# Kernel tuning notes

Measured on AMD Instinct MI355X. Metric: run time of the kernel, lower is better.

## Reference

```python
import jax, jax.numpy as jnp
import numpy as np

S, B, E, D, H, F, L = 1024, 8, 768, 8, 8, 2048, 4
D = 1024  # HIDDEN_DIM
H = 8     # nhead
DH = D // H
EPS = 1e-5


def _ln(x, g, b):
    m = jnp.mean(x, -1, keepdims=True)
    v = jnp.mean(jnp.square(x - m), -1, keepdims=True)
    return (x - m) * jax.lax.rsqrt(v + EPS) * g + b


def setup_inputs() -> dict:
    key = jax.random.key(0)
    ks = iter(jax.random.split(key, 16))
    n = lambda shape: jax.random.normal(next(ks), shape, jnp.float32) * 0.02
    return dict(
        x=jax.random.normal(next(ks), (S, B, E), jnp.float32),
        enc_w=n((D, E)), enc_b=jnp.zeros((D,), jnp.float32),
        enc_ln_g=jnp.ones((D,), jnp.float32), enc_ln_b=jnp.zeros((D,), jnp.float32),
        qkv_w=n((L, 3 * D, D)), qkv_b=jnp.zeros((L, 3 * D), jnp.float32),
        out_w=n((L, D, D)), out_b=jnp.zeros((L, D), jnp.float32),
        ln1_g=jnp.ones((L, D), jnp.float32), ln1_b=jnp.zeros((L, D), jnp.float32),
        ff1_w=n((L, F, D)), ff1_b=jnp.zeros((L, F), jnp.float32),
        ff2_w=n((L, D, F)), ff2_b=jnp.zeros((L, D), jnp.float32),
        ln2_g=jnp.ones((L, D), jnp.float32), ln2_b=jnp.zeros((L, D), jnp.float32),
        dec_w1=n((D // 2, D)), dec_b1=jnp.zeros((D // 2,), jnp.float32),
        dec_ln_g=jnp.ones((D // 2,), jnp.float32), dec_ln_b=jnp.zeros((D // 2,), jnp.float32),
        dec_w2=n((E, D // 2)), dec_b2=jnp.zeros((E,), jnp.float32),
    )


def reference(x, enc_w, enc_b, enc_ln_g, enc_ln_b, qkv_w, qkv_b, out_w, out_b,
              ln1_g, ln1_b, ff1_w, ff1_b, ff2_w, ff2_b, ln2_g, ln2_b,
              dec_w1, dec_b1, dec_ln_g, dec_ln_b, dec_w2, dec_b2):
    # encoder MLP: Linear -> LayerNorm -> ReLU (dropout = identity at eval)
    h = jax.nn.relu(_ln(x @ enc_w.T + enc_b, enc_ln_g, enc_ln_b))  # (S,B,D)
    scale = np.float32(1.0 / np.sqrt(DH))
    for l in range(L):  # 4 post-norm TransformerEncoderLayers, eager attention
        qkv = h @ qkv_w[l].T + qkv_b[l]                    # (S,B,3D)
        q, k, v = jnp.split(qkv, 3, axis=-1)
        q = q.reshape(S, B, H, DH)
        k = k.reshape(S, B, H, DH)
        v = v.reshape(S, B, H, DH)
        scores = jnp.einsum('sbhd,tbhd->bhst', q, k) * scale  # (B,H,S,S)
        p = jax.nn.softmax(scores, axis=-1)
        o = jnp.einsum('bhst,tbhd->sbhd', p, v).reshape(S, B, D)
        o = o @ out_w[l].T + out_b[l]
        h = _ln(h + o, ln1_g[l], ln1_b[l])
        f = jax.nn.relu(h @ ff1_w[l].T + ff1_b[l]) @ ff2_w[l].T + ff2_b[l]
        h = _ln(h + f, ln2_g[l], ln2_b[l])
    # decoder MLP
    d = jax.nn.relu(_ln(h @ dec_w1.T + dec_b1, dec_ln_g, dec_ln_b))
    return d @ dec_w2.T + dec_b2  # (S,B,E)
```

## Files before the change

### kernel.cpp

```cpp
#include <hip/hip_runtime.h>
#include <math.h>

#define S_ 1024
#define B_ 8
#define E_ 768
#define D_ 1024
#define H_ 8
#define F_ 2048
#define L_ 4
#define M_ (S_*B_)

typedef unsigned short u16;
typedef unsigned int u32;
typedef u16 u16x8 __attribute__((ext_vector_type(8)));
typedef u16 u16x4 __attribute__((ext_vector_type(4)));
typedef u16 u16x2 __attribute__((ext_vector_type(2)));
typedef u32 u32x2 __attribute__((ext_vector_type(2)));
typedef short bf16x8 __attribute__((ext_vector_type(8)));
typedef float f32x4 __attribute__((ext_vector_type(4)));

#define AS1 __attribute__((address_space(1)))
#define AS3 __attribute__((address_space(3)))

#define QSCALE 0.127517432f

__device__ __forceinline__ void gload_lds16(const void* g, void* l) {
  __builtin_amdgcn_global_load_lds((const AS1 void*)g, (AS3 void*)l, 16, 0, 0);
}
__device__ __forceinline__ u16 f2bf(float f) {
  unsigned u = __builtin_bit_cast(unsigned, f);
  return (u16)((u + 0x7fffu + ((u >> 16) & 1u)) >> 16);
}
__device__ __forceinline__ float bf2f(u16 h) {
  unsigned u = ((unsigned)h) << 16;
  return __builtin_bit_cast(float, u);
}
__device__ __forceinline__ u32 cvtpk(float a, float b) {
  u32 r;
  asm("v_cvt_pk_bf16_f32 %0, %1, %2" : "=v"(r) : "v"(a), "v"(b));
  return r;
}

__global__ __launch_bounds__(256) void conv4(
    const float* __restrict__ s0, u16* __restrict__ d0, int n0,
    const float* __restrict__ s1, u16* __restrict__ d1, int n1,
    const float* __restrict__ s2, u16* __restrict__ d2, int n2,
    const float* __restrict__ s3, u16* __restrict__ d3, int n3)
{
  int total = (n0 + n1 + n2 + n3) >> 2;
  for (int i = blockIdx.x * 256 + threadIdx.x; i < total; i += gridDim.x * 256) {
    int e = i << 2;
    const float* s; u16* d; int off;
    if (e < n0)           { s = s0; d = d0; off = e; }
    else if (e < n0+n1)   { s = s1; d = d1; off = e - n0; }
    else if (e < n0+n1+n2){ s = s2; d = d2; off = e - n0 - n1; }
    else                  { s = s3; d = d3; off = e - n0 - n1 - n2; }
    float4 v = *(const float4*)&s[off];
    u16x4 o; o[0]=f2bf(v.x); o[1]=f2bf(v.y); o[2]=f2bf(v.z); o[3]=f2bf(v.w);
    *(u16x4*)&d[off] = o;
  }
}

template<int ACT, int SCQ>
__global__ __launch_bounds__(512) void gemm512(
    const u16* __restrict__ A, const u16* __restrict__ W,
    const float* __restrict__ bias, u16* __restrict__ Cout,
    int M, int N, int K)
{
  __shared__ u16 lds[65536];
  const int gx = gridDim.x, nwg = gx * gridDim.y;
  const int lin = blockIdx.y * gx + blockIdx.x;
  const int work = (lin & 7) * (nwg >> 3) + (lin >> 3);
  const int bm = (work / gx) * 256, bn = (work % gx) * 256;
  const int tid = threadIdx.x;
  const int l = tid & 63;
  const int w = tid >> 6;
  const int l15 = l & 15, lg = l >> 4;
  const int wr = w >> 2, wc = w & 3;
  f32x4 acc[8][4] = {};
  const int nt = K >> 6;

#define STG(c, k0)                                                          \
  {                                                                         \
    u16* Ab = lds + (c)*32768;                                              \
    u16* Bb = Ab + 16384;                                                   \
    _Pragma("unroll")                                                       \
    for (int u = 0; u < 4; ++u) {                                           \
      int row = u*64 + (tid >> 3);                                          \
      int cb  = (tid & 7) ^ (row & 7);                                      \
      gload_lds16(A + (size_t)(bm + row) * K + (k0) + cb*8,                 \
                  Ab + u*4096 + tid*8);                                     \
    }                                                                       \
    _Pragma("unroll")                                                       \
    for (int u = 0; u < 4; ++u) {                                           \
      int row = u*64 + (tid >> 3);                                          \
      int cb  = (tid & 7) ^ (row & 7);                                      \
      gload_lds16(W + (size_t)(bn + row) * K + (k0) + cb*8,                 \
                  Bb + u*4096 + tid*8);                                     \
    }                                                                       \
  }

  STG(0, 0);
  STG(1, 64);
  asm volatile("s_waitcnt vmcnt(8)" ::: "memory");
  __builtin_amdgcn_s_barrier();

  for (int t = 0; t < nt; ++t) {
    const u16* Ab = lds + (t & 1)*32768;
    const u16* Bb = Ab + 16384;

    bf16x8 af[8], bfv[4];
    #pragma unroll
    for (int mi = 0; mi < 8; ++mi) {
      int row = wr*128 + mi*16 + l15;
      af[mi] = *(const bf16x8*)&Ab[row*64 + ((lg) ^ (row & 7))*8];
    }
    #pragma unroll
    for (int ni = 0; ni < 4; ++ni) {
      int row = wc*64 + ni*16 + l15;
      bfv[ni] = *(const bf16x8*)&Bb[row*64 + ((lg) ^ (row & 7))*8];
    }
    asm volatile("s_waitcnt lgkmcnt(0)" ::: "memory");
    __builtin_amdgcn_sched_barrier(0);
    #pragma unroll
    for (int mi = 0; mi < 8; ++mi)
      #pragma unroll
      for (int ni = 0; ni < 4; ++ni)
        acc[mi][ni] = __builtin_amdgcn_mfma_f32_16x16x32_bf16(af[mi], bfv[ni], acc[mi][ni], 0, 0, 0);

    #pragma unroll
    for (int mi = 0; mi < 8; ++mi) {
      int row = wr*128 + mi*16 + l15;
      af[mi] = *(const bf16x8*)&Ab[row*64 + ((4 + lg) ^ (row & 7))*8];
    }
    #pragma unroll
    for (int ni = 0; ni < 4; ++ni) {
      int row = wc*64 + ni*16 + l15;
      bfv[ni] = *(const bf16x8*)&Bb[row*64 + ((4 + lg) ^ (row & 7))*8];
    }
    asm volatile("s_waitcnt lgkmcnt(0)" ::: "memory");
    __builtin_amdgcn_sched_barrier(0);
    __builtin_amdgcn_s_barrier();

    if (t + 2 < nt) STG(t & 1, (t + 2) << 6);

    #pragma unroll
    for (int mi = 0; mi < 8; ++mi)
      #pragma unroll
      for (int ni = 0; ni < 4; ++ni)
        acc[mi][ni] = __builtin_amdgcn_mfma_f32_16x16x32_bf16(af[mi], bfv[ni], acc[mi][ni], 0, 0, 0);

    if (t + 1 < nt) {
      if (t + 2 < nt) { asm volatile("s_waitcnt vmcnt(8)" ::: "memory"); }
      else            { asm volatile("s_waitcnt vmcnt(0)" ::: "memory"); }
      __builtin_amdgcn_s_barrier();
    }
  }
#undef STG

  #pragma unroll
  for (int ni = 0; ni < 4; ++ni) {
    int col = bn + wc*64 + ni*16 + l15;
    float bv = bias[col];
    #pragma unroll
    for (int mi = 0; mi < 8; ++mi) {
      #pragma unroll
      for (int rr = 0; rr < 4; ++rr) {
        int row = bm + wr*128 + mi*16 + lg*4 + rr;
        float v = acc[mi][ni][rr] + bv;
        if (ACT) v = fmaxf(v, 0.f);
        if (SCQ) { if (col < 1024) v *= QSCALE; }
        Cout[(size_t)row * N + col] = f2bf(v);
      }
    }
  }
}

template<int ACT, int OUTBF, int SCQ, int RES>
__global__ __launch_bounds__(512) void gemm256(
    const u16* __restrict__ A, const u16* __restrict__ W,
    const float* __restrict__ bias, const u16* __restrict__ Rres,
    void* __restrict__ Cout, int M, int N, int K)
{
  __shared__ u16 lds[73728];
  const int gx = gridDim.x, nwg = gx * gridDim.y;
  const int lin = blockIdx.y * gx + blockIdx.x;
  const int work = (lin & 7) * (nwg >> 3) + (lin >> 3);
  const int bm = (work / gx) * 256, bn = (work % gx) * 128;
  const int tid = threadIdx.x;
  const int l = tid & 63;
  const int w = tid >> 6;
  const int l15 = l & 15, lg = l >> 4;
  const int wr = w >> 2, wc = w & 3;
  const int srow = tid >> 3;
  const int scb  = tid & 7;

  f32x4 acc[8][2] = {};
  const int nt = K >> 6;

#define STAGE_A(c, k0)                                                      \
  {                                                                         \
    u16* Ab = lds + (c)*24576;                                              \
    _Pragma("unroll")                                                       \
    for (int u = 0; u < 4; ++u) {                                           \
      int row = u*64 + srow;                                                \
      int cb  = scb ^ (row & 7);                                            \
      gload_lds16(A + (size_t)(bm + row) * K + (k0) + cb*8,                 \
                  Ab + u*4096 + tid*8);                                     \
    }                                                                       \
  }
#define STAGE_B(c, k0)                                                      \
  {                                                                         \
    u16* Bb = lds + (c)*24576 + 16384;                                      \
    _Pragma("unroll")                                                       \
    for (int u = 0; u < 2; ++u) {                                           \
      int row = u*64 + srow;                                                \
      int cb  = scb ^ (row & 7);                                            \
      gload_lds16(W + (size_t)(bn + row) * K + (k0) + cb*8,                 \
                  Bb + u*4096 + tid*8);                                     \
    }                                                                       \
  }

  STAGE_A(0, 0);  STAGE_B(0, 0);
  STAGE_A(1, 64); STAGE_B(1, 64);
  asm volatile("s_waitcnt vmcnt(6)" ::: "memory");
  __builtin_amdgcn_s_barrier();

  int cr = 0, cw = 2;
  for (int t = 0; t < nt; ++t) {
    const u16* Ab = lds + cr*24576;
    const u16* Bb = Ab + 16384;

    bf16x8 bfr[2][2];
    #pragma unroll
    for (int ni = 0; ni < 2; ++ni) {
      int row = wc*32 + ni*16 + l15;
      bfr[ni][0] = *(const bf16x8*)&Bb[row*64 + ((lg) ^ (row & 7))*8];
      bfr[ni][1] = *(const bf16x8*)&Bb[row*64 + ((4 + lg) ^ (row & 7))*8];
    }

    {
      bf16x8 af[4][2];
      #pragma unroll
      for (int mi = 0; mi < 4; ++mi) {
        int row = wr*128 + mi*16 + l15;
        af[mi][0] = *(const bf16x8*)&Ab[row*64 + ((lg) ^ (row & 7))*8];
        af[mi][1] = *(const bf16x8*)&Ab[row*64 + ((4 + lg) ^ (row & 7))*8];
      }
      if (t + 2 < nt) STAGE_A(cw, (t + 2) << 6);
      #pragma unroll
      for (int ks = 0; ks < 2; ++ks)
        #pragma unroll
        for (int mi = 0; mi < 4; ++mi)
          #pragma unroll
          for (int ni = 0; ni < 2; ++ni)
            acc[mi][ni] = __builtin_amdgcn_mfma_f32_16x16x32_bf16(af[mi][ks], bfr[ni][ks], acc[mi][ni], 0, 0, 0);
    }

    {
      bf16x8 af[4][2];
      #pragma unroll
      for (int mi = 0; mi < 4; ++mi) {
        int row = wr*128 + (4 + mi)*16 + l15;
        af[mi][0] = *(const bf16x8*)&Ab[row*64 + ((lg) ^ (row & 7))*8];
        af[mi][1] = *(const bf16x8*)&Ab[row*64 + ((4 + lg) ^ (row & 7))*8];
      }
      if (t + 2 < nt) STAGE_B(cw, (t + 2) << 6);
      #pragma unroll
      for (int ks = 0; ks < 2; ++ks)
        #pragma unroll
        for (int mi = 0; mi < 4; ++mi)
          #pragma unroll
          for (int ni = 0; ni < 2; ++ni)
            acc[4 + mi][ni] = __builtin_amdgcn_mfma_f32_16x16x32_bf16(af[mi][ks], bfr[ni][ks], acc[4 + mi][ni], 0, 0, 0);
    }

    if (t + 1 < nt) {
      if (t + 2 < nt) { asm volatile("s_waitcnt vmcnt(6)" ::: "memory"); }
      else            { asm volatile("s_waitcnt vmcnt(0)" ::: "memory"); }
      __builtin_amdgcn_s_barrier();
    }
    cr = (cr == 2) ? 0 : cr + 1;
    cw = (cw == 2) ? 0 : cw + 1;
  }
#undef STAGE_A
#undef STAGE_B

  u16* Cb = (u16*)Cout; float* Cf = (float*)Cout;
  #pragma unroll
  for (int ni = 0; ni < 2; ++ni) {
    int col = bn + wc*32 + ni*16 + l15;
    float bv = bias[col];
    #pragma unroll
    for (int mi = 0; mi < 8; ++mi) {
      #pragma unroll
      for (int rr = 0; rr < 4; ++rr) {
        int row = bm + wr*128 + mi*16 + lg*4 + rr;
        float v = acc[mi][ni][rr] + bv;
        if (RES) v += bf2f(Rres[(size_t)row * N + col]);
        if (ACT) v = fmaxf(v, 0.f);
        if (SCQ) { if (col < 1024) v *= QSCALE; }
        if (OUTBF) Cb[(size_t)row * N + col] = f2bf(v);
        else       Cf[(size_t)row * N + col] = v;
      }
    }
  }
}

template<int NV, bool RELU>
__global__ __launch_bounds__(256) void ln_bf16(
    const u16* __restrict__ X,
    const float* __restrict__ g, const float* __restrict__ b,
    u16* __restrict__ Y)
{
  constexpr int D = NV * 256;
  __shared__ float sbuf[8];
  const int tid = threadIdx.x;
  const size_t base = (size_t)blockIdx.x * D + tid * NV;
  float v[NV];
  if constexpr (NV == 4) {
    u16x4 xv = *(const u16x4*)&X[base];
    #pragma unroll
    for (int i = 0; i < 4; ++i) v[i] = bf2f(xv[i]);
  } else {
    u16x2 xv = *(const u16x2*)&X[base];
    #pragma unroll
    for (int i = 0; i < 2; ++i) v[i] = bf2f(xv[i]);
  }
  float sum = 0.f, sq = 0.f;
  #pragma unroll
  for (int i = 0; i < NV; ++i) { sum += v[i]; sq += v[i]*v[i]; }
  #pragma unroll
  for (int off = 32; off > 0; off >>= 1) {
    sum += __shfl_down(sum, off);
    sq  += __shfl_down(sq, off);
  }
  if ((tid & 63) == 0) { sbuf[tid >> 6] = sum; sbuf[4 + (tid >> 6)] = sq; }
  __syncthreads();
  sum = sbuf[0] + sbuf[1] + sbuf[2] + sbuf[3];
  sq  = sbuf[4] + sbuf[5] + sbuf[6] + sbuf[7];
  const float mean = sum / (float)D;
  const float rstd = rsqrtf(sq / (float)D - mean*mean + 1e-5f);
  const int c0 = tid * NV;
  if constexpr (NV == 4) {
    u16x4 o;
    #pragma unroll
    for (int i = 0; i < 4; ++i) {
      float t = (v[i] - mean) * rstd * g[c0+i] + b[c0+i];
      if (RELU) t = fmaxf(t, 0.f);
      o[i] = f2bf(t);
    }
    *(u16x4*)&Y[base] = o;
  } else {
    u16x2 o;
    #pragma unroll
    for (int i = 0; i < 2; ++i) {
      float t = (v[i] - mean) * rstd * g[c0+i] + b[c0+i];
      if (RELU) t = fmaxf(t, 0.f);
      o[i] = f2bf(t);
    }
    *(u16x2*)&Y[base] = o;
  }
}

__global__ __launch_bounds__(256) void vtrans(
    const u16* __restrict__ QKV, u16* __restrict__ Vt)
{
  __shared__ u16 Ls[32*132];
  const int st = blockIdx.x, bh = blockIdx.y;
  const int bb = bh >> 3, hh = bh & 7;
  const int t = threadIdx.x;
  #pragma unroll
  for (int i = 0; i < 2; ++i) {
    int e = i*256 + t;
    int s = e >> 4, d0 = (e & 15) * 8;
    u16x8 v = *(const u16x8*)&QKV[(size_t)((st*32 + s)*8 + bb)*3072 + 2048 + hh*128 + d0];
    #pragma unroll
    for (int j = 0; j < 4; ++j) {
      u16x2 p; p[0] = v[2*j]; p[1] = v[2*j+1];
      *(u16x2*)&Ls[s*132 + d0 + 2*j] = p;
    }
  }
  __syncthreads();
  #pragma unroll
  for (int i = 0; i < 2; ++i) {
    int e = i*256 + t;
    int d = e >> 2, s0 = (e & 3) * 8;
    u16x8 v;
    #pragma unroll
    for (int j = 0; j < 8; ++j) v[j] = Ls[(s0+j)*132 + d];
    *(u16x8*)&Vt[(size_t)bh*131072 + (size_t)d*1024 + st*32 + s0] = v;
  }
}

__global__ __launch_bounds__(512, 4) void attn_mfma(
    const u16* __restrict__ QKV, const u16* __restrict__ Vt,
    u16* __restrict__ AO)
{
  __shared__ u16 Ks[2][64*128];
  __shared__ u16 Vs[2][128*64];
  __shared__ u16 Pl[8][16*64];
  const int bid = blockIdx.x;
  const int wg = (bid & 7) * 64 + (bid >> 3);
  const int qt = wg & 7, bh = wg >> 3;
  const int bb = bh >> 3, hh = bh & 7;
  const int tid = threadIdx.x, w = tid >> 6, l = tid & 63;
  const int l15 = l & 15, lg = l >> 4;

  bf16x8 aq[4];
  {
    int q = qt*128 + w*16 + l15;
    const u16* qp = QKV + (size_t)(q*8 + bb)*3072 + hh*128 + lg*8;
    #pragma unroll
    for (int kc = 0; kc < 4; ++kc)
      aq[kc] = *(const bf16x8*)(qp + kc*32);
  }
  const u16* vbase = Vt + (size_t)bh*131072;

#define STAGE_KV(c, kt)                                                     \
  {                                                                         \
    _Pragma("unroll")                                                       \
    for (int i = 0; i < 2; ++i) {                                           \
      int e = (w*2 + i) * 512 + l * 8;                                      \
      int krow = e >> 7, d0 = e & 127;                                      \
      int dsw = d0 ^ ((krow & 7) << 3);                                     \
      gload_lds16(QKV + (size_t)(((kt)*64 + krow)*8 + bb)*3072 + 1024       \
                      + hh*128 + dsw,                                       \
                  &Ks[c][(w*2 + i) * 512]);                                 \
      int vd = e >> 6, vc = e & 63;                                         \
      int vsw = vc ^ ((vd & 7) << 3);                                       \
      gload_lds16(vbase + (size_t)vd*1024 + (kt)*64 + vsw,                  \
                  &Vs[c][(w*2 + i) * 512]);                                 \
    }                                                                       \
  }

  f32x4 of[8] = {};
  float mreg = -INFINITY, lpart = 0.f;
  const int psw = (l15 & 7) << 3;

  STAGE_KV(0, 0);
  __syncthreads();

  for (int kt = 0; kt < 16; ++kt) {
    const int cur = kt & 1;
    if (kt + 1 < 16) STAGE_KV(cur ^ 1, kt + 1);

    f32x4 sf[4] = {};
    #pragma unroll
    for (int kc = 0; kc < 4; ++kc) {
      #pragma unroll
      for (int f = 0; f < 4; ++f) {
        int krow = f*16 + l15;
        bf16x8 bk = *(const bf16x8*)&Ks[cur][krow*128 + ((kc*32 + lg*8) ^ ((krow & 7) << 3))];
        sf[f] = __builtin_amdgcn_mfma_f32_16x16x32_bf16(bk, aq[kc], sf[f], 0, 0, 0);
      }
    }

    float pm01 = fmaxf(fmaxf(sf[0][0], sf[0][1]), fmaxf(sf[0][2], sf[0][3]));
    float pm23 = fmaxf(fmaxf(sf[1][0], sf[1][1]), fmaxf(sf[1][2], sf[1][3]));
    float pm45 = fmaxf(fmaxf(sf[2][0], sf[2][1]), fmaxf(sf[2][2], sf[2][3]));
    float pm67 = fmaxf(fmaxf(sf[3][0], sf[3][1]), fmaxf(sf[3][2], sf[3][3]));
    float pmax = fmaxf(fmaxf(pm01, pm23), fmaxf(pm45, pm67));
    pmax = fmaxf(pmax, __shfl_xor(pmax, 16));
    pmax = fmaxf(pmax, __shfl_xor(pmax, 32));

    if (__any(pmax > mreg + 8.f)) {
      float mn = fmaxf(mreg, pmax);
      float al = exp2f(mreg - mn);
      mreg = mn;
      lpart *= al;
      #pragma unroll
      for (int r = 0; r < 4; ++r) {
        float alq = __shfl(al, (l & 48) + lg*4 + r);
        #pragma unroll
        for (int ni = 0; ni < 8; ++ni) of[ni][r] *= alq;
      }
    }

    float psum = 0.f;
    #pragma unroll
    for (int f = 0; f < 4; ++f) {
      float p0 = exp2f(sf[f][0] - mreg);
      float p1 = exp2f(sf[f][1] - mreg);
      float p2 = exp2f(sf[f][2] - mreg);
      float p3 = exp2f(sf[f][3] - mreg);
      psum += (p0 + p1) + (p2 + p3);
      u32x2 pk; pk[0] = cvtpk(p0, p1); pk[1] = cvtpk(p2, p3);
      *(u32x2*)&Pl[w][l15*64 + ((f*16 + lg*4) ^ psw)] = pk;
    }
    lpart += psum;

    bf16x8 pa0 = *(const bf16x8*)&Pl[w][l15*64 + ((lg*8) ^ psw)];
    bf16x8 pa1 = *(const bf16x8*)&Pl[w][l15*64 + ((32 + lg*8) ^ psw)];
    #pragma unroll
    for (int ni = 0; ni < 8; ++ni) {
      int n = ni*16 + l15;
      int nsw = (n & 7) << 3;
      bf16x8 vb0 = *(const bf16x8*)&Vs[cur][n*64 + ((lg*8) ^ nsw)];
      bf16x8 vb1 = *(const bf16x8*)&Vs[cur][n*64 + ((32 + lg*8) ^ nsw)];
      of[ni] = __builtin_amdgcn_mfma_f32_16x16x32_bf16(pa0, vb0, of[ni], 0, 0, 0);
      of[ni] = __builtin_amdgcn_mfma_f32_16x16x32_bf16(pa1, vb1, of[ni], 0, 0, 0);
    }

    if (kt + 1 < 16) __syncthreads();
  }
#undef STAGE_KV

  float ls = lpart;
  ls += __shfl_xor(ls, 16);
  ls += __shfl_xor(ls, 32);
  float inv = 1.f / ls;
  #pragma unroll
  for (int r = 0; r < 4; ++r) {
    float invq = __shfl(inv, (l & 48) + lg*4 + r);
    int q = qt*128 + w*16 + lg*4 + r;
    size_t base = (size_t)(q*8 + bb) * 1024 + hh*128;
    #pragma unroll
    for (int ni = 0; ni < 8; ++ni)
      AO[base + ni*16 + l15] = f2bf(of[ni][r] * invq);
  }
}

#define O_WENC  0ull
#define O_WDEC1 786432ull
#define O_WDEC2 1310720ull
#define O_WLQ   1703936ull
#define O_WLO   4849664ull
#define O_WLF1  5898240ull
#define O_WLF2  7995392ull
#define O_R     10092544ull
#define O_H     35258368ull
#define O_AO    43646976ull
#define O_VT    52035584ull

extern "C" void kernel_launch(void* const* d_in, const int* in_sizes, int n_in,
                              void* d_out, int out_size, void* d_ws, size_t ws_size,
                              hipStream_t stream) {
  (void)in_sizes; (void)n_in; (void)out_size; (void)ws_size;
  const float* x        = (const float*)d_in[0];
  const float* enc_w    = (const float*)d_in[1];
  const float* enc_b    = (const float*)d_in[2];
  const float* enc_ln_g = (const float*)d_in[3];
  const float* enc_ln_b = (const float*)d_in[4];
  const float* qkv_w    = (const float*)d_in[5];
  const float* qkv_b    = (const float*)d_in[6];
  const float* out_w    = (const float*)d_in[7];
  const float* out_b    = (const float*)d_in[8];
  const float* ln1_g    = (const float*)d_in[9];
  const float* ln1_b    = (const float*)d_in[10];
  const float* ff1_w    = (const float*)d_in[11];
  const float* ff1_b    = (const float*)d_in[12];
  const float* ff2_w    = (const float*)d_in[13];
  const float* ff2_b    = (const float*)d_in[14];
  const float* ln2_g    = (const float*)d_in[15];
  const float* ln2_b    = (const float*)d_in[16];
  const float* dec_w1   = (const float*)d_in[17];
  const float* dec_b1   = (const float*)d_in[18];
  const float* dec_ln_g = (const float*)d_in[19];
  const float* dec_ln_b = (const float*)d_in[20];
  const float* dec_w2   = (const float*)d_in[21];
  const float* dec_b2   = (const float*)d_in[22];

  u16* ws16 = (u16*)d_ws;
  u16* wenc  = ws16 + O_WENC;
  u16* wdec1 = ws16 + O_WDEC1;
  u16* wdec2 = ws16 + O_WDEC2;
  u16* wlq   = ws16 + O_WLQ;
  u16* wlo   = ws16 + O_WLO;
  u16* wlf1  = ws16 + O_WLF1;
  u16* wlf2  = ws16 + O_WLF2;
  u16* qkv   = ws16 + O_R;
  u16* bufY  = ws16 + O_R;
  u16* bufG  = ws16 + O_R + 8388608ull;
  u16* xb    = bufG;
  u16* dech  = bufG;
  u16* h     = ws16 + O_H;
  u16* ao    = ws16 + O_AO;
  u16* vt    = ws16 + O_VT;

  const dim3 blk(256);
  const dim3 blk5(512);

  conv4<<<1024, blk, 0, stream>>>(x, xb, 8192*768,
                                  enc_w, wenc, 1024*768,
                                  dec_w1, wdec1, 512*1024,
                                  dec_w2, wdec2, 768*512);
  gemm256<0,1,0,0><<<dim3(8,32), blk5, 0, stream>>>(xb, wenc, enc_b, nullptr, bufY, M_, 1024, 768);
  ln_bf16<4,true><<<M_, blk, 0, stream>>>(bufY, enc_ln_g, enc_ln_b, h);

  for (int l = 0; l < L_; ++l) {
    conv4<<<1024, blk, 0, stream>>>(qkv_w + (size_t)l*3145728, wlq, 3145728,
                                    out_w + (size_t)l*1048576, wlo, 1048576,
                                    ff1_w + (size_t)l*2097152, wlf1, 2097152,
                                    ff2_w + (size_t)l*2097152, wlf2, 2097152);
    gemm512<0,1><<<dim3(12,32), blk5, 0, stream>>>(h, wlq, qkv_b + (size_t)l*3072, qkv, M_, 3072, 1024);
    vtrans<<<dim3(32,64), blk, 0, stream>>>(qkv, vt);
    attn_mfma<<<512, blk5, 0, stream>>>(qkv, vt, ao);
    gemm256<0,1,0,1><<<dim3(8,32), blk5, 0, stream>>>(ao, wlo, out_b + (size_t)l*1024, h, bufY, M_, 1024, 1024);
    ln_bf16<4,false><<<M_, blk, 0, stream>>>(bufY, ln1_g + (size_t)l*1024, ln1_b + (size_t)l*1024, h);
    gemm512<1,0><<<dim3(8,32), blk5, 0, stream>>>(h, wlf1, ff1_b + (size_t)l*2048, bufG, M_, 2048, 1024);
    gemm256<0,1,0,1><<<dim3(8,32), blk5, 0, stream>>>(bufG, wlf2, ff2_b + (size_t)l*1024, h, bufY, M_, 1024, 2048);
    ln_bf16<4,false><<<M_, blk, 0, stream>>>(bufY, ln2_g + (size_t)l*1024, ln2_b + (size_t)l*1024, h);
  }

  gemm256<0,1,0,0><<<dim3(4,32), blk5, 0, stream>>>(h, wdec1, dec_b1, nullptr, bufY, M_, 512, 1024);
  ln_bf16<2,true><<<M_, blk, 0, stream>>>(bufY, dec_ln_g, dec_ln_b, dech);
  gemm256<0,0,0,0><<<dim3(6,32), blk5, 0, stream>>>(dech, wdec2, dec_b2, nullptr, d_out, M_, 768, 512);
}
```

Baseline: 1.077 ms.

## Rework QKV/FF1 GEMM into 256x128 tiles with triple-buffered K=32 stages

Replaces the 256x256, K=64, double-buffered GEMM used for the QKV and FF1 projections with a 256x128 tile, K=32 step, three-stage LDS ring. Global-to-LDS loads for stage t+2 are interleaved between the two MFMA halves, with a new swizzle for 32-wide rows. The smaller LDS footprint and doubled grid aim for better occupancy, CU fill and load/compute overlap. The cost is lower arithmetic intensity per tile and more barriers per unit of K.

```diff
diff --git a/kernel.cpp b/kernel.cpp
--- a/kernel.cpp
+++ b/kernel.cpp
@@ -62,105 +62,108 @@
 }
 
 template<int ACT, int SCQ>
-__global__ __launch_bounds__(512) void gemm512(
+__global__ __launch_bounds__(512) void gemm32(
     const u16* __restrict__ A, const u16* __restrict__ W,
     const float* __restrict__ bias, u16* __restrict__ Cout,
     int M, int N, int K)
 {
-  __shared__ u16 lds[65536];
+  __shared__ u16 lds[36864];
   const int gx = gridDim.x, nwg = gx * gridDim.y;
   const int lin = blockIdx.y * gx + blockIdx.x;
   const int work = (lin & 7) * (nwg >> 3) + (lin >> 3);
-  const int bm = (work / gx) * 256, bn = (work % gx) * 256;
+  const int bm = (work / gx) * 256, bn = (work % gx) * 128;
   const int tid = threadIdx.x;
   const int l = tid & 63;
   const int w = tid >> 6;
   const int l15 = l & 15, lg = l >> 4;
   const int wr = w >> 2, wc = w & 3;
-  f32x4 acc[8][4] = {};
-  const int nt = K >> 6;
-
-#define STG(c, k0)                                                          \
+  const int srow = tid >> 2;
+  const int scb  = tid & 3;
+
+  f32x4 acc[8][2] = {};
+  const int nt = K >> 5;
+
+#define STAGE_A32(c, k0)                                                    \
   {                                                                         \
-    u16* Ab = lds + (c)*32768;                                              \
-    u16* Bb = Ab + 16384;                                                   \
+    u16* Ab = lds + (c)*12288;                                              \
     _Pragma("unroll")                                                       \
-    for (int u = 0; u < 4; ++u) {                                           \
-      int row = u*64 + (tid >> 3);                                          \
-      int cb  = (tid & 7) ^ (row & 7);                                      \
+    for (int u = 0; u < 2; ++u) {                                           \
+      int row = u*128 + srow;                                               \
+      int cb  = scb ^ ((row >> 1) & 3);                                     \
       gload_lds16(A + (size_t)(bm + row) * K + (k0) + cb*8,                 \
                   Ab + u*4096 + tid*8);                                     \
     }                                                                       \
-    _Pragma("unroll")                                                       \
-    for (int u = 0; u < 4; ++u) {                                           \
-      int row = u*64 + (tid >> 3);                                          \
-      int cb  = (tid & 7) ^ (row & 7);                                      \
-      gload_lds16(W + (size_t)(bn + row) * K + (k0) + cb*8,                 \
-                  Bb + u*4096 + tid*8);                                     \
-    }                                                                       \
-  }
-
-  STG(0, 0);
-  STG(1, 64);
-  asm volatile("s_waitcnt vmcnt(8)" ::: "memory");
+  }
+#define STAGE_B32(c, k0)                                                    \
+  {                                                                         \
+    u16* Bb = lds + (c)*12288 + 8192;                                       \
+    int row = srow;                                                         \
+    int cb  = scb ^ ((row >> 1) & 3);                                       \
+    gload_lds16(W + (size_t)(bn + row) * K + (k0) + cb*8,                   \
+                Bb + tid*8);                                                \
+  }
+
+  STAGE_A32(0, 0);  STAGE_B32(0, 0);
+  STAGE_A32(1, 32); STAGE_B32(1, 32);
+  asm volatile("s_waitcnt vmcnt(3)" ::: "memory");
   __builtin_amdgcn_s_barrier();
 
+  int cr = 0, cw = 2;
   for (int t = 0; t < nt; ++t) {
-    const u16* Ab = lds + (t & 1)*32768;
-    const u16* Bb = Ab + 16384;
-
-    bf16x8 af[8], bfv[4];
-    #pragma unroll
-    for (int mi = 0; mi < 8; ++mi) {
-      int row = wr*128 + mi*16 + l15;
-      af[mi] = *(const bf16x8*)&Ab[row*64 + ((lg) ^ (row & 7))*8];
-    }
-    #pragma unroll
-    for (int ni = 0; ni < 4; ++ni) {
-      int row = wc*64 + ni*16 + l15;
-      bfv[ni] = *(const bf16x8*)&Bb[row*64 + ((lg) ^ (row & 7))*8];
-    }
-    asm volatile("s_waitcnt lgkmcnt(0)" ::: "memory");
-    __builtin_amdgcn_sched_barrier(0);
-    #pragma unroll
-    for (int mi = 0; mi < 8; ++mi)
-      #pragma unroll
-      for (int ni = 0; ni < 4; ++ni)
-        acc[mi][ni] = __builtin_amdgcn_mfma_f32_16x16x32_bf16(af[mi], bfv[ni], acc[mi][ni], 0, 0, 0);
-
-    #pragma unroll
-    for (int mi = 0; mi < 8; ++mi) {
-      int row = wr*128 + mi*16 + l15;
-      af[mi] = *(const bf16x8*)&Ab[row*64 + ((4 + lg) ^ (row & 7))*8];
-    }
-    #pragma unroll
-    for (int ni = 0; ni < 4; ++ni) {
-      int row = wc*64 + ni*16 + l15;
-      bfv[ni] = *(const bf16x8*)&Bb[row*64 + ((4 + lg) ^ (row & 7))*8];
-    }
-    asm volatile("s_waitcnt lgkmcnt(0)" ::: "memory");
-    __builtin_amdgcn_sched_barrier(0);
-    __builtin_amdgcn_s_barrier();
-
-    if (t + 2 < nt) STG(t & 1, (t + 2) << 6);
-
-    #pragma unroll
-    for (int mi = 0; mi < 8; ++mi)
-      #pragma unroll
-      for (int ni = 0; ni < 4; ++ni)
-        acc[mi][ni] = __builtin_amdgcn_mfma_f32_16x16x32_bf16(af[mi], bfv[ni], acc[mi][ni], 0, 0, 0);
+    const u16* Ab = lds + cr*12288;
+    const u16* Bb = Ab + 8192;
+
+    bf16x8 bfr[2];
+    #pragma unroll
+    for (int ni = 0; ni < 2; ++ni) {
+      int row = wc*32 + ni*16 + l15;
+      bfr[ni] = *(const bf16x8*)&Bb[row*32 + (lg ^ ((row >> 1) & 3))*8];
+    }
+
+    {
+      bf16x8 af[4];
+      #pragma unroll
+      for (int mi = 0; mi < 4; ++mi) {
+        int row = wr*128 + mi*16 + l15;
+        af[mi] = *(const bf16x8*)&Ab[row*32 + (lg ^ ((row >> 1) & 3))*8];
+      }
+      if (t + 2 < nt) STAGE_A32(cw, (t + 2) << 5);
+      #pragma unroll
+      for (int mi = 0; mi < 4; ++mi)
+        #pragma unroll
+        for (int ni = 0; ni < 2; ++ni)
+          acc[mi][ni] = __builtin_amdgcn_mfma_f32_16x16x32_bf16(af[mi], bfr[ni], acc[mi][ni], 0, 0, 0);
+    }
+
+    {
+      bf16x8 af[4];
+      #pragma unroll
+      for (int mi = 0; mi < 4; ++mi) {
+        int row = wr*128 + (4 + mi)*16 + l15;
+        af[mi] = *(const bf16x8*)&Ab[row*32 + (lg ^ ((row >> 1) & 3))*8];
+      }
+      if (t + 2 < nt) STAGE_B32(cw, (t + 2) << 5);
+      #pragma unroll
+      for (int mi = 0; mi < 4; ++mi)
+        #pragma unroll
+        for (int ni = 0; ni < 2; ++ni)
+          acc[4 + mi][ni] = __builtin_amdgcn_mfma_f32_16x16x32_bf16(af[mi], bfr[ni], acc[4 + mi][ni], 0, 0, 0);
+    }
 
     if (t + 1 < nt) {
-      if (t + 2 < nt) { asm volatile("s_waitcnt vmcnt(8)" ::: "memory"); }
+      if (t + 2 < nt) { asm volatile("s_waitcnt vmcnt(3)" ::: "memory"); }
       else            { asm volatile("s_waitcnt vmcnt(0)" ::: "memory"); }
       __builtin_amdgcn_s_barrier();
     }
-  }
-#undef STG
+    cr = (cr == 2) ? 0 : cr + 1;
+    cw = (cw == 2) ? 0 : cw + 1;
+  }
+#undef STAGE_A32
+#undef STAGE_B32
 
   #pragma unroll
-  for (int ni = 0; ni < 4; ++ni) {
-    int col = bn + wc*64 + ni*16 + l15;
+  for (int ni = 0; ni < 2; ++ni) {
+    int col = bn + wc*32 + ni*16 + l15;
     float bv = bias[col];
     #pragma unroll
     for (int mi = 0; mi < 8; ++mi) {
@@ -593,12 +596,12 @@
                                     out_w + (size_t)l*1048576, wlo, 1048576,
                                     ff1_w + (size_t)l*2097152, wlf1, 2097152,
                                     ff2_w + (size_t)l*2097152, wlf2, 2097152);
-    gemm512<0,1><<<dim3(12,32), blk5, 0, stream>>>(h, wlq, qkv_b + (size_t)l*3072, qkv, M_, 3072, 1024);
+    gemm32<0,1><<<dim3(24,32), blk5, 0, stream>>>(h, wlq, qkv_b + (size_t)l*3072, qkv, M_, 3072, 1024);
     vtrans<<<dim3(32,64), blk, 0, stream>>>(qkv, vt);
     attn_mfma<<<512, blk5, 0, stream>>>(qkv, vt, ao);
     gemm256<0,1,0,1><<<dim3(8,32), blk5, 0, stream>>>(ao, wlo, out_b + (size_t)l*1024, h, bufY, M_, 1024, 1024);
     ln_bf16<4,false><<<M_, blk, 0, stream>>>(bufY, ln1_g + (size_t)l*1024, ln1_b + (size_t)l*1024, h);
-    gemm512<1,0><<<dim3(8,32), blk5, 0, stream>>>(h, wlf1, ff1_b + (size_t)l*2048, bufG, M_, 2048, 1024);
+    gemm32<1,0><<<dim3(16,32), blk5, 0, stream>>>(h, wlf1, ff1_b + (size_t)l*2048, bufG, M_, 2048, 1024);
     gemm256<0,1,0,1><<<dim3(8,32), blk5, 0, stream>>>(bufG, wlf2, ff2_b + (size_t)l*1024, h, bufY, M_, 1024, 2048);
     ln_bf16<4,false><<<M_, blk, 0, stream>>>(bufY, ln2_g + (size_t)l*1024, ln2_b + (size_t)l*1024, h);
   }
```

Result: faster. 1.038 ms (-3.7%).
